# Kernel tuning notes

Measured on AMD Instinct MI355X. Metric: run time of the kernel, lower is better.

Reference implementation:

```python
import jax, jax.numpy as jnp
import numpy as np

EMBED = 1024
HEADS = 16
HEAD_DIM = EMBED // HEADS

def setup_inputs() -> dict:
    key = jax.random.key(0)
    ks = jax.random.split(key, 9)
    N, Q, K = 2, 2048, 2048
    queries = jax.random.normal(ks[0], (N, Q, EMBED), dtype=jnp.float32)
    keys_ = jax.random.normal(ks[1], (N, K, EMBED), dtype=jnp.float32)
    values = jax.random.normal(ks[2], (N, K, EMBED), dtype=jnp.float32)
    mask = jax.random.randint(ks[3], (N, 1, Q, K), 0, 2, dtype=jnp.int32)
    s = 1.0 / np.sqrt(EMBED)
    Wq = jax.random.normal(ks[4], (EMBED, EMBED), dtype=jnp.float32) * s
    Wk = jax.random.normal(ks[5], (EMBED, EMBED), dtype=jnp.float32) * s
    Wv = jax.random.normal(ks[6], (EMBED, EMBED), dtype=jnp.float32) * s
    Wo = jax.random.normal(ks[7], (EMBED, EMBED), dtype=jnp.float32) * s
    bo = jax.random.normal(ks[8], (EMBED,), dtype=jnp.float32) * s
    return {"queries": queries, "keys": keys_, "values": values, "mask": mask,
            "Wq": Wq, "Wk": Wk, "Wv": Wv, "Wo": Wo, "bo": bo}

def reference(queries, keys, values, mask, Wq, Wk, Wv, Wo, bo):
    N, Qlen, _ = queries.shape
    Klen = keys.shape[1]
    # Linear projections (torch Linear: x @ W.T), then split heads
    q = (queries @ Wq.T).reshape(N, Qlen, HEADS, HEAD_DIM)
    k = (keys @ Wk.T).reshape(N, Klen, HEADS, HEAD_DIM)
    v = (values @ Wv.T).reshape(N, Klen, HEADS, HEAD_DIM)
    energy = jnp.einsum('nqhd,nkhd->nhqk', q, k)  # [N,H,Q,K]
    energy = jnp.where(mask == 0, jnp.float32(-1e20), energy)
    # NOTE: original scales by sqrt(embed_size), not sqrt(head_dim)
    attention = jax.nn.softmax(energy / jnp.sqrt(jnp.float32(EMBED)), axis=3)
    out = jnp.einsum('nhqk,nkhd->nqhd', attention, v).reshape(N, Qlen, EMBED)
    return out @ Wo.T + bo
```

## Files before the change

### kernel.cpp

```cpp
#include <hip/hip_runtime.h>
#include <stdint.h>
#include <stddef.h>

typedef __attribute__((ext_vector_type(8)))  short bf16x8;
typedef __attribute__((ext_vector_type(2)))  float f32x2;
typedef __attribute__((ext_vector_type(4)))  float f32x4;
typedef __attribute__((ext_vector_type(16))) float f32x16;
typedef __attribute__((ext_vector_type(4)))  float float4v;
typedef __attribute__((ext_vector_type(4)))  int   int4v;

#define DEV static __device__ __forceinline__

static constexpr int EMBED  = 1024;
static constexpr int HEADS  = 16;
static constexpr int SEQ    = 2048;

DEV short f2bf(float f) {
  union { float f; unsigned u; } x; x.f = f;
  unsigned r = x.u + 0x7fffu + ((x.u >> 16) & 1u);
  return (short)(r >> 16);
}

DEV int cvtpk(float a, float b) {
  int r; asm("v_cvt_pk_bf16_f32 %0, %1, %2" : "=v"(r) : "v"(a), "v"(b)); return r;
}

DEV float fexp2(float x) { float r; asm("v_exp_f32 %0, %1" : "=v"(r) : "v"(x)); return r; }

#define MFMA16(a,b,c) __builtin_amdgcn_mfma_f32_16x16x32_bf16((a),(b),(c),0,0,0)
#define MFMA32(a,b,c) __builtin_amdgcn_mfma_f32_32x32x16_bf16((a),(b),(c),0,0,0)
#define GLDS(g,l) __builtin_amdgcn_global_load_lds( \
    (const __attribute__((address_space(1))) void*)(g), \
    (__attribute__((address_space(3))) void*)(l), 16, 0, 0)
#define SBAR0() __builtin_amdgcn_sched_barrier(0)
#define ZERO16 {0,0,0,0,0,0,0,0,0,0,0,0,0,0,0,0}


struct CvtArgs { const float* src[7]; short* dst[7]; int n[7]; };

__global__ void cvt_bf16(CvtArgs a) {
  const int task = blockIdx.y;
  const int i = (blockIdx.x * 256 + threadIdx.x) * 8;
  if (i >= a.n[task]) return;
  const float4v* s = (const float4v*)(a.src[task] + i);
  float4v x = s[0], y = s[1];
  bf16x8 o;
  o[0] = f2bf(x[0]); o[1] = f2bf(x[1]); o[2] = f2bf(x[2]); o[3] = f2bf(x[3]);
  o[4] = f2bf(y[0]); o[5] = f2bf(y[1]); o[6] = f2bf(y[2]); o[7] = f2bf(y[3]);
  *(bf16x8*)(a.dst[task] + i) = o;
}

__global__ void maskpack(const int* __restrict__ m, unsigned long long* __restrict__ out) {
  const int gw = (blockIdx.x * 256 + threadIdx.x) >> 6;
  const int l  = threadIdx.x & 63;
  const int n = gw >> 16, kvblk = (gw >> 11) & 31, q = gw & 2047;
  int v = m[((size_t)n * SEQ + q) * SEQ + kvblk * 64 + l];
  unsigned long long b = __ballot(v != 0);
  if (l == 0) out[((size_t)n * 32 + kvblk) * SEQ + q] = b;
}

template<int MODE>
DEV void gemm_core(const int vv, const short* __restrict__ A, const short* __restrict__ B,
                   short* __restrict__ Cb, float* __restrict__ Cf,
                   const float* __restrict__ bias, short* As, short* Bs)
{
  const int t = threadIdx.x;
  const int l = t & 63, w = t >> 6;
  const int lr = l & 15, lh = l >> 4;
  const int m0 = (vv >> 3) * 128, n0 = (vv & 7) * 128;
  const int wr = w >> 1, wc = w & 1;
  f32x4 acc[4][4] = {};

  const int rA = t >> 2, cA = (t & 3) * 8;
  const short* gA  = A + (size_t)(m0 + rA) * 1024 + cA;
  const short* gA2 = gA + (size_t)64 * 1024;
  const short* gB  = B + (size_t)(n0 + rA) * 1024 + cA;
  const short* gB2 = gB + (size_t)64 * 1024;

  GLDS(gA,  As + w * 512);
  GLDS(gA2, As + 2048 + w * 512);
  GLDS(gB,  Bs + w * 512);
  GLDS(gB2, Bs + 2048 + w * 512);

  #pragma unroll 1
  for (int it = 0; it < 32; ++it) {
    if (it < 31) {
      const int nb = (it + 1) & 1;
      const int kt = (it + 1) * 32;
      GLDS(gA + kt,  As + nb * 4096 + w * 512);
      GLDS(gA2 + kt, As + nb * 4096 + 2048 + w * 512);
      GLDS(gB + kt,  Bs + nb * 4096 + w * 512);
      GLDS(gB2 + kt, Bs + nb * 4096 + 2048 + w * 512);
      asm volatile("s_waitcnt vmcnt(4)" ::: "memory");
      SBAR0();
    } else {
      asm volatile("s_waitcnt vmcnt(0)" ::: "memory");
      SBAR0();
    }
    __builtin_amdgcn_s_barrier();
    SBAR0();

    const short* as = As + (it & 1) * 4096;
    const short* bs = Bs + (it & 1) * 4096;
    bf16x8 af[4], bq[4];
    #pragma unroll
    for (int i = 0; i < 4; ++i)
      af[i] = *(const bf16x8*)&as[(wr * 64 + i * 16 + lr) * 32 + lh * 8];
    #pragma unroll
    for (int i = 0; i < 4; ++i)
      bq[i] = *(const bf16x8*)&bs[(wc * 64 + i * 16 + lr) * 32 + lh * 8];
    #pragma unroll
    for (int mi = 0; mi < 4; ++mi)
      #pragma unroll
      for (int ni = 0; ni < 4; ++ni)
        acc[mi][ni] = MFMA16(af[mi], bq[ni], acc[mi][ni]);

    SBAR0();
    __builtin_amdgcn_s_barrier();
    SBAR0();
  }

  #pragma unroll
  for (int mi = 0; mi < 4; ++mi)
    #pragma unroll
    for (int ni = 0; ni < 4; ++ni)
      #pragma unroll
      for (int r = 0; r < 4; ++r) {
        const int m = m0 + wr * 64 + mi * 16 + lh * 4 + r;
        const int e = n0 + wc * 64 + ni * 16 + lr;
        const float v = acc[mi][ni][r];
        const int nb = m >> 11, s = m & 2047, hh = e >> 6, d = e & 63;
        if (MODE == 0) {
          Cb[(((size_t)(nb * HEADS + hh)) * SEQ + s) * 64 + d] = f2bf(v);
        } else if (MODE == 2) {
          Cb[(((size_t)(nb * HEADS + hh)) * SEQ + s) * 64 + (d ^ ((s & 7) << 3))] = f2bf(v);
        } else if (MODE == 3) {
          Cb[(((size_t)(nb * HEADS + hh)) * 32 + (s >> 6)) * 4096 + d * 64 +
             ((s & 63) ^ ((d & 7) << 3))] = f2bf(v);
        } else {
          Cf[(size_t)m * EMBED + e] = v + bias[e];
        }
      }
}

__global__ __launch_bounds__(256, 2)
void gemm_qkv(const short* __restrict__ Ab, const short* __restrict__ Bb,
              short* __restrict__ Qp, short* __restrict__ Kp, short* __restrict__ VTp)
{
  __shared__ short As[2][4096];
  __shared__ short Bs[2][4096];
  const int lin = blockIdx.x;
  const int s = lin >> 8, j = lin & 255;
  const int vv = (j & 7) * 32 + (j >> 3);
  const short* A = Ab + (size_t)s * 4194304;
  const short* B = Bb + (size_t)s * 1048576;
  if (s == 0)      gemm_core<0>(vv, A, B, Qp,  nullptr, nullptr, &As[0][0], &Bs[0][0]);
  else if (s == 1) gemm_core<2>(vv, A, B, Kp,  nullptr, nullptr, &As[0][0], &Bs[0][0]);
  else             gemm_core<3>(vv, A, B, VTp, nullptr, nullptr, &As[0][0], &Bs[0][0]);
}

__global__ __launch_bounds__(256, 2)
void gemm_out(const short* __restrict__ A, const short* __restrict__ B,
              float* __restrict__ Cf, const float* __restrict__ bias)
{
  __shared__ short As[2][4096];
  __shared__ short Bs[2][4096];
  const int lin = blockIdx.x;
  const int vv = (lin & 7) * 32 + (lin >> 3);
  gemm_core<1>(vv, A, B, nullptr, Cf, bias, &As[0][0], &Bs[0][0]);
}

__global__ __launch_bounds__(256, 2)
void attn256(const short* __restrict__ Qp, const short* __restrict__ Kp,
             const short* __restrict__ VTp, const unsigned long long* __restrict__ MbT,
             short* __restrict__ Aout)
{
  __shared__ short lds[2][8192];

  const int t = threadIdx.x, l = t & 63, w = t >> 6;
  const int lq = l & 31, hi = l >> 5;
  const int lin = blockIdx.x;
  const int vv = (lin & 7) * 64 + (lin >> 3);
  const int hl = vv >> 4, qb = vv & 15;
  const int n = hl >> 4, h = hl & 15;
  const int q0 = qb * 128;
  const int myq = q0 + w * 32 + lq;
  const size_t hb = (size_t)(n * HEADS + h) * SEQ * 64;
  const short* Qh = Qp + hb;
  const short* Kh = Kp + hb;
  const short* Vh = VTp + hb;
  const unsigned long long* Mh = MbT + (size_t)n * (32 * SEQ);
  const float SCL = 0.045084220027780106f;

  bf16x8 qf[4];
  #pragma unroll
  for (int ks = 0; ks < 4; ++ks)
    qf[ks] = *(const bf16x8*)(Qh + (size_t)myq * 64 + ks * 16 + hi * 8);

  const short ONE = (short)0x3F80;
  const bf16x8 onesv = {ONE, ONE, ONE, ONE, ONE, ONE, ONE, ONE};
  const f32x16 zerov = ZERO16;

  f32x16 acco[2] = { ZERO16, ZERO16 };
  f32x16 accl = ZERO16;

  unsigned long long mw = Mh[myq];
  {
    const short* Kt = Kh + w * 1024 + l * 8;
    const short* Vt = Vh + w * 1024 + l * 8;
    GLDS(Kt,       &lds[0][w * 1024]);
    GLDS(Kt + 512, &lds[0][w * 1024 + 512]);
    GLDS(Vt,       &lds[0][4096 + w * 1024]);
    GLDS(Vt + 512, &lds[0][4096 + w * 1024 + 512]);
  }

  #pragma unroll 1
  for (int tt = 0; tt < 32; ++tt) {
    unsigned long long mw_next = 0;
    if (tt < 31) {
      mw_next = Mh[(size_t)(tt + 1) * SEQ + myq];
      SBAR0();
      const int nb = (tt + 1) & 1;
      const short* Kt = Kh + (size_t)(tt + 1) * 4096 + w * 1024 + l * 8;
      const short* Vt = Vh + (size_t)(tt + 1) * 4096 + w * 1024 + l * 8;
      GLDS(Kt,       &lds[nb][w * 1024]);
      GLDS(Kt + 512, &lds[nb][w * 1024 + 512]);
      GLDS(Vt,       &lds[nb][4096 + w * 1024]);
      GLDS(Vt + 512, &lds[nb][4096 + w * 1024 + 512]);
      asm volatile("s_waitcnt vmcnt(5)" ::: "memory");
      SBAR0();
    } else {
      asm volatile("s_waitcnt vmcnt(0)" ::: "memory");
      SBAR0();
    }
    __builtin_amdgcn_s_barrier();
    SBAR0();

    const short* Ks  = &lds[tt & 1][0];
    const short* VTs = &lds[tt & 1][4096];

    #pragma unroll
    for (int half = 0; half < 2; ++half) {
      f32x16 sacc;
      __builtin_amdgcn_s_setprio(1);
      #pragma unroll
      for (int ks = 0; ks < 4; ++ks) {
        const int d = ks * 16 + hi * 8;
        bf16x8 kf = *(const bf16x8*)&Ks[(half * 32 + lq) * 64 + (d ^ ((lq & 7) << 3))];
        sacc = MFMA32(kf, qf[ks], ks == 0 ? zerov : sacc);
      }
      __builtin_amdgcn_s_setprio(0);
      const unsigned mmw = ~(unsigned)(mw >> (half * 32 + hi * 4));
      float p[16];
      #pragma unroll
      for (int r = 0; r < 16; ++r) {
        const int idx = (r & 3) + 8 * (r >> 2);
        union { int i; float f; } b;
        b.i = __builtin_amdgcn_sbfe(mmw, idx, 1) & 0xC3480000;
        p[r] = fexp2(__builtin_fmaf(sacc[r], SCL, b.f));
      }
      bf16x8 pf[2];
      #pragma unroll
      for (int kb = 0; kb < 2; ++kb) {
        int x1 = cvtpk(p[kb * 8 + 0], p[kb * 8 + 1]);
        int y1 = cvtpk(p[kb * 8 + 4], p[kb * 8 + 5]);
        int x2 = cvtpk(p[kb * 8 + 2], p[kb * 8 + 3]);
        int y2 = cvtpk(p[kb * 8 + 6], p[kb * 8 + 7]);
        asm("v_permlane32_swap_b32 %0, %1" : "+v"(x1), "+v"(y1));
        asm("v_permlane32_swap_b32 %0, %1" : "+v"(x2), "+v"(y2));
        union { int w4[4]; bf16x8 v; } u;
        u.w4[0] = x1; u.w4[1] = x2; u.w4[2] = y1; u.w4[3] = y2;
        pf[kb] = u.v;
      }
      __builtin_amdgcn_s_setprio(1);
      accl = MFMA32(onesv, pf[0], accl);
      accl = MFMA32(onesv, pf[1], accl);
      #pragma unroll
      for (int dt = 0; dt < 2; ++dt) {
        const int d = dt * 32 + lq;
        #pragma unroll
        for (int kb = 0; kb < 2; ++kb) {
          const int kv = half * 32 + kb * 16 + hi * 8;
          bf16x8 vf = *(const bf16x8*)&VTs[d * 64 + (kv ^ ((d & 7) << 3))];
          acco[dt] = MFMA32(vf, pf[kb], acco[dt]);
        }
      }
      __builtin_amdgcn_s_setprio(0);
    }
    mw = mw_next;
    SBAR0();
    __builtin_amdgcn_s_barrier();
    SBAR0();
  }

  const float invs = 1.f / (accl[0] + 1e-30f);

  short* ot = &lds[0][0] + w * 2048;
  #pragma unroll
  for (int dt = 0; dt < 2; ++dt)
    #pragma unroll
    for (int r = 0; r < 16; ++r) {
      const int d = dt * 32 + (r & 3) + 8 * (r >> 2) + 4 * hi;
      ot[lq * 64 + (d ^ ((lq & 7) << 3))] = f2bf(acco[dt][r] * invs);
    }
  __syncthreads();

  const int qq = l >> 1, hb2 = l & 1;
  #pragma unroll
  for (int it = 0; it < 4; ++it) {
    const int didx = (hb2 * 32 + it * 8) ^ ((qq & 7) << 3);
    bf16x8 v = *(const bf16x8*)&ot[qq * 64 + didx];
    *(bf16x8*)&Aout[((size_t)(n * SEQ + q0 + w * 32 + qq)) * EMBED + h * 64 + hb2 * 32 + it * 8] = v;
  }
}

extern "C" void kernel_launch(void* const* d_in, const int* in_sizes, int n_in,
                              void* d_out, int out_size, void* d_ws, size_t ws_size,
                              hipStream_t stream) {
  (void)in_sizes; (void)n_in; (void)out_size;
  const float* queries = (const float*)d_in[0];
  const float* keys    = (const float*)d_in[1];
  const float* values  = (const float*)d_in[2];
  const int*   mask    = (const int*)d_in[3];
  const float* Wq      = (const float*)d_in[4];
  const float* Wk      = (const float*)d_in[5];
  const float* Wv      = (const float*)d_in[6];
  const float* Wo      = (const float*)d_in[7];
  const float* bo      = (const float*)d_in[8];

  const size_t NEED = (size_t)76 * 1024 * 1024;
  if (ws_size < NEED) return;

  char* ws = (char*)d_ws;
  short* qb   = (short*)(ws + 0);
  short* kb   = (short*)(ws + (8u << 20));
  short* vb   = (short*)(ws + (16u << 20));
  short* wqb  = (short*)(ws + (24u << 20));
  short* wkb  = (short*)(ws + (26u << 20));
  short* wvb  = (short*)(ws + (28u << 20));
  short* wob  = (short*)(ws + (30u << 20));
  unsigned long long* mbits = (unsigned long long*)(ws + (32u << 20));
  short* Qp   = (short*)(ws + (40u << 20));
  short* Kp   = (short*)(ws + (48u << 20));
  short* VTp  = (short*)(ws + (56u << 20));
  short* ao   = (short*)(ws + (64u << 20));

  const int NTOK = 2 * SEQ * EMBED;
  const int NW   = EMBED * EMBED;

  CvtArgs ca;
  ca.src[0] = queries; ca.dst[0] = qb;  ca.n[0] = NTOK;
  ca.src[1] = keys;    ca.dst[1] = kb;  ca.n[1] = NTOK;
  ca.src[2] = values;  ca.dst[2] = vb;  ca.n[2] = NTOK;
  ca.src[3] = Wq;      ca.dst[3] = wqb; ca.n[3] = NW;
  ca.src[4] = Wk;      ca.dst[4] = wkb; ca.n[4] = NW;
  ca.src[5] = Wv;      ca.dst[5] = wvb; ca.n[5] = NW;
  ca.src[6] = Wo;      ca.dst[6] = wob; ca.n[6] = NW;
  cvt_bf16<<<dim3(2048, 7), 256, 0, stream>>>(ca);

  maskpack<<<dim3(32768), 256, 0, stream>>>(mask, mbits);

  gemm_qkv<<<dim3(768), 256, 0, stream>>>(qb, wqb, Qp, Kp, VTp);

  attn256<<<dim3(512), 256, 0, stream>>>(Qp, Kp, VTp, mbits, ao);

  gemm_out<<<dim3(256), 256, 0, stream>>>(ao, wob, (float*)d_out, bo);
}
```

Measured before the change: 144.3 us.

## Triple-buffer LDS tiles in GEMM and attention loops, dropping the trailing barrier

Both the GEMM core and the attention kernel go from double-buffered to triple-buffered LDS tiles. Loads are now issued two iterations ahead, after a single barrier per iteration, and the end-of-iteration barrier is removed. The aim is to hide more global-load latency and halve per-iteration synchronisation. The cost is a larger LDS footprint (48KB per block), which could limit occupancy, and more careful vmcnt accounting.

```diff
diff --git a/kernel.cpp b/kernel.cpp
--- a/kernel.cpp
+++ b/kernel.cpp
@@ -34,6 +34,7 @@
     (__attribute__((address_space(3))) void*)(l), 16, 0, 0)
 #define SBAR0() __builtin_amdgcn_sched_barrier(0)
 #define ZERO16 {0,0,0,0,0,0,0,0,0,0,0,0,0,0,0,0}
+#define ROT3(x) ((x) == 2 ? 0 : (x) + 1)
 
 
 struct CvtArgs { const float* src[7]; short* dst[7]; int n[7]; };
@@ -77,31 +78,36 @@
   const short* gB  = B + (size_t)(n0 + rA) * 1024 + cA;
   const short* gB2 = gB + (size_t)64 * 1024;
 
-  GLDS(gA,  As + w * 512);
-  GLDS(gA2, As + 2048 + w * 512);
-  GLDS(gB,  Bs + w * 512);
-  GLDS(gB2, Bs + 2048 + w * 512);
-
+  GLDS(gA,       As + w * 512);
+  GLDS(gA2,      As + 2048 + w * 512);
+  GLDS(gB,       Bs + w * 512);
+  GLDS(gB2,      Bs + 2048 + w * 512);
+  SBAR0();
+  GLDS(gA + 32,  As + 4096 + w * 512);
+  GLDS(gA2 + 32, As + 4096 + 2048 + w * 512);
+  GLDS(gB + 32,  Bs + 4096 + w * 512);
+  GLDS(gB2 + 32, Bs + 4096 + 2048 + w * 512);
+  SBAR0();
+
+  int cb = 0, sb = 2;
   #pragma unroll 1
   for (int it = 0; it < 32; ++it) {
-    if (it < 31) {
-      const int nb = (it + 1) & 1;
-      const int kt = (it + 1) * 32;
-      GLDS(gA + kt,  As + nb * 4096 + w * 512);
-      GLDS(gA2 + kt, As + nb * 4096 + 2048 + w * 512);
-      GLDS(gB + kt,  Bs + nb * 4096 + w * 512);
-      GLDS(gB2 + kt, Bs + nb * 4096 + 2048 + w * 512);
-      asm volatile("s_waitcnt vmcnt(4)" ::: "memory");
+    if (it < 31) { asm volatile("s_waitcnt vmcnt(4)" ::: "memory"); }
+    else         { asm volatile("s_waitcnt vmcnt(0)" ::: "memory"); }
+    SBAR0();
+    __builtin_amdgcn_s_barrier();
+    SBAR0();
+    if (it < 30) {
+      const int kt = (it + 2) * 32;
+      GLDS(gA + kt,  As + sb * 4096 + w * 512);
+      GLDS(gA2 + kt, As + sb * 4096 + 2048 + w * 512);
+      GLDS(gB + kt,  Bs + sb * 4096 + w * 512);
+      GLDS(gB2 + kt, Bs + sb * 4096 + 2048 + w * 512);
       SBAR0();
-    } else {
-      asm volatile("s_waitcnt vmcnt(0)" ::: "memory");
-      SBAR0();
-    }
-    __builtin_amdgcn_s_barrier();
-    SBAR0();
-
-    const short* as = As + (it & 1) * 4096;
-    const short* bs = Bs + (it & 1) * 4096;
+    }
+
+    const short* as = As + cb * 4096;
+    const short* bs = Bs + cb * 4096;
     bf16x8 af[4], bq[4];
     #pragma unroll
     for (int i = 0; i < 4; ++i)
@@ -116,8 +122,7 @@
         acc[mi][ni] = MFMA16(af[mi], bq[ni], acc[mi][ni]);
 
     SBAR0();
-    __builtin_amdgcn_s_barrier();
-    SBAR0();
+    cb = ROT3(cb); sb = ROT3(sb);
   }
 
   #pragma unroll
@@ -147,8 +152,8 @@
 void gemm_qkv(const short* __restrict__ Ab, const short* __restrict__ Bb,
               short* __restrict__ Qp, short* __restrict__ Kp, short* __restrict__ VTp)
 {
-  __shared__ short As[2][4096];
-  __shared__ short Bs[2][4096];
+  __shared__ short As[3][4096];
+  __shared__ short Bs[3][4096];
   const int lin = blockIdx.x;
   const int s = lin >> 8, j = lin & 255;
   const int vv = (j & 7) * 32 + (j >> 3);
@@ -163,8 +168,8 @@
 void gemm_out(const short* __restrict__ A, const short* __restrict__ B,
               float* __restrict__ Cf, const float* __restrict__ bias)
 {
-  __shared__ short As[2][4096];
-  __shared__ short Bs[2][4096];
+  __shared__ short As[3][4096];
+  __shared__ short Bs[3][4096];
   const int lin = blockIdx.x;
   const int vv = (lin & 7) * 32 + (lin >> 3);
   gemm_core<1>(vv, A, B, nullptr, Cf, bias, &As[0][0], &Bs[0][0]);
@@ -175,7 +180,7 @@
              const short* __restrict__ VTp, const unsigned long long* __restrict__ MbT,
              short* __restrict__ Aout)
 {
-  __shared__ short lds[2][8192];
+  __shared__ short lds[3][8192];
 
   const int t = threadIdx.x, l = t & 63, w = t >> 6;
   const int lq = l & 31, hi = l >> 5;
@@ -187,8 +192,6 @@
   const int myq = q0 + w * 32 + lq;
   const size_t hb = (size_t)(n * HEADS + h) * SEQ * 64;
   const short* Qh = Qp + hb;
-  const short* Kh = Kp + hb;
-  const short* Vh = VTp + hb;
   const unsigned long long* Mh = MbT + (size_t)n * (32 * SEQ);
   const float SCL = 0.045084220027780106f;
 
@@ -204,40 +207,49 @@
   f32x16 acco[2] = { ZERO16, ZERO16 };
   f32x16 accl = ZERO16;
 
-  unsigned long long mw = Mh[myq];
-  {
-    const short* Kt = Kh + w * 1024 + l * 8;
-    const short* Vt = Vh + w * 1024 + l * 8;
-    GLDS(Kt,       &lds[0][w * 1024]);
-    GLDS(Kt + 512, &lds[0][w * 1024 + 512]);
-    GLDS(Vt,       &lds[0][4096 + w * 1024]);
-    GLDS(Vt + 512, &lds[0][4096 + w * 1024 + 512]);
-  }
-
+  const short* kgp = Kp + hb + w * 1024 + l * 8;
+  const short* vgp = VTp + hb + w * 1024 + l * 8;
+  const unsigned long long* mp = MbT + (size_t)n * (32 * SEQ) + myq;
+
+  unsigned long long mw = *mp; mp += SEQ;
+  SBAR0();
+  GLDS(kgp,        &lds[0][w * 1024]);
+  GLDS(kgp + 512,  &lds[0][w * 1024 + 512]);
+  GLDS(vgp,        &lds[0][4096 + w * 1024]);
+  GLDS(vgp + 512,  &lds[0][4096 + w * 1024 + 512]);
+  SBAR0();
+  GLDS(kgp + 4096, &lds[1][w * 1024]);
+  GLDS(kgp + 4608, &lds[1][w * 1024 + 512]);
+  GLDS(vgp + 4096, &lds[1][4096 + w * 1024]);
+  GLDS(vgp + 4608, &lds[1][4096 + w * 1024 + 512]);
+  SBAR0();
+  kgp += 8192; vgp += 8192;
+
+  int cb = 0, sb = 2;
   #pragma unroll 1
   for (int tt = 0; tt < 32; ++tt) {
+    if (tt < 31) { asm volatile("s_waitcnt vmcnt(4)" ::: "memory"); }
+    else         { asm volatile("s_waitcnt vmcnt(0)" ::: "memory"); }
+    SBAR0();
+    __builtin_amdgcn_s_barrier();
+    SBAR0();
+
     unsigned long long mw_next = 0;
     if (tt < 31) {
-      mw_next = Mh[(size_t)(tt + 1) * SEQ + myq];
+      mw_next = *mp; mp += SEQ;
       SBAR0();
-      const int nb = (tt + 1) & 1;
-      const short* Kt = Kh + (size_t)(tt + 1) * 4096 + w * 1024 + l * 8;
-      const short* Vt = Vh + (size_t)(tt + 1) * 4096 + w * 1024 + l * 8;
-      GLDS(Kt,       &lds[nb][w * 1024]);
-      GLDS(Kt + 512, &lds[nb][w * 1024 + 512]);
-      GLDS(Vt,       &lds[nb][4096 + w * 1024]);
-      GLDS(Vt + 512, &lds[nb][4096 + w * 1024 + 512]);
-      asm volatile("s_waitcnt vmcnt(5)" ::: "memory");
+    }
+    if (tt < 30) {
+      GLDS(kgp,       &lds[sb][w * 1024]);
+      GLDS(kgp + 512, &lds[sb][w * 1024 + 512]);
+      GLDS(vgp,       &lds[sb][4096 + w * 1024]);
+      GLDS(vgp + 512, &lds[sb][4096 + w * 1024 + 512]);
+      kgp += 4096; vgp += 4096;
       SBAR0();
-    } else {
-      asm volatile("s_waitcnt vmcnt(0)" ::: "memory");
-      SBAR0();
-    }
-    __builtin_amdgcn_s_barrier();
-    SBAR0();
-
-    const short* Ks  = &lds[tt & 1][0];
-    const short* VTs = &lds[tt & 1][4096];
+    }
+
+    const short* Ks  = &lds[cb][0];
+    const short* VTs = &lds[cb][4096];
 
     #pragma unroll
     for (int half = 0; half < 2; ++half) {
@@ -289,8 +301,7 @@
     }
     mw = mw_next;
     SBAR0();
-    __builtin_amdgcn_s_barrier();
-    SBAR0();
+    cb = ROT3(cb); sb = ROT3(sb);
   }
 
   const float invs = 1.f / (accl[0] + 1e-30f);
```

Result: no change. 146.5 us (+1.5%).
